# Performance work log

Hardware: AMD Instinct MI355X
Metric: run time of the kernel (lower is better)

Reference implementation:

```python
import jax, jax.numpy as jnp
import numpy as np

I = 1739   # input/output feature size (num_nodes)
H = 256    # hidden size
T = 2048   # trajectory length


def gru(x_seq, h0, W_ih, W_hh, b_ih, b_hh):
    """PyTorch-convention GRU over x_seq [T, I] with h0 [H]. Returns (hs [T,H], h_T [H])."""
    x_proj = x_seq @ W_ih.T + b_ih  # [T, 3H], precompute input projections

    def step(h, xp):
        hh = h @ W_hh.T + b_hh  # [3H]
        xr, xz, xn = xp[:H], xp[H:2 * H], xp[2 * H:]
        hr, hz, hn = hh[:H], hh[H:2 * H], hh[2 * H:]
        r = jax.nn.sigmoid(xr + hr)
        z = jax.nn.sigmoid(xz + hz)
        n = jnp.tanh(xn + r * hn)
        h_new = (1.0 - z) * n + z * h
        return h_new, h_new

    h_T, hs = jax.lax.scan(step, h0, x_proj)
    return hs, h_T


def setup_inputs() -> dict:
    key = jax.random.key(0)
    ks = jax.random.split(key, 12)
    s = 1.0 / np.sqrt(H)
    inp = {
        "input_trajectory": jax.random.normal(ks[0], (1, T, I), jnp.float32),
        "target_trajectory": jax.random.normal(ks[1], (1, T, I), jnp.float32),
        "W_ih_enc": jax.random.uniform(ks[2], (3 * H, I), jnp.float32, -s, s),
        "W_hh_enc": jax.random.uniform(ks[3], (3 * H, H), jnp.float32, -s, s),
        "b_ih_enc": jax.random.uniform(ks[4], (3 * H,), jnp.float32, -s, s),
        "b_hh_enc": jax.random.uniform(ks[5], (3 * H,), jnp.float32, -s, s),
        "W_ih_dec": jax.random.uniform(ks[6], (3 * H, I), jnp.float32, -s, s),
        "W_hh_dec": jax.random.uniform(ks[7], (3 * H, H), jnp.float32, -s, s),
        "b_ih_dec": jax.random.uniform(ks[8], (3 * H,), jnp.float32, -s, s),
        "b_hh_dec": jax.random.uniform(ks[9], (3 * H,), jnp.float32, -s, s),
        "W_out": jax.random.uniform(ks[10], (I, H), jnp.float32, -s, s),
        "b_out": jax.random.uniform(ks[11], (I,), jnp.float32, -s, s),
    }
    return inp


def reference(input_trajectory, target_trajectory,
              W_ih_enc, W_hh_enc, b_ih_enc, b_hh_enc,
              W_ih_dec, W_hh_dec, b_ih_dec, b_hh_dec,
              W_out, b_out):
    x = input_trajectory[0]  # [T, I], batch=1
    h0 = jnp.zeros((H,), x.dtype)
    # Encoder: only the final hidden state is used.
    _, h_enc = gru(x, h0, W_ih_enc, W_hh_enc, b_ih_enc, b_hh_enc)
    # Decoder: loop feeds each input timestep through a 1-step GRU;
    # this is exactly a GRU over the full sequence starting from h_enc.
    hs, _ = gru(x, h_enc, W_ih_dec, W_hh_dec, b_ih_dec, b_hh_dec)  # [T, H]
    # Per-step Linear is a single batched matmul over all steps.
    preds = hs @ W_out.T + b_out  # [T, I]
    # Original cats per-step (1,1,I) tensors along dim=0 -> [T, 1, I].
    return preds[:, None, :]
```

## Files before the change

### kernel.cpp

```cpp
#include <hip/hip_runtime.h>
#include <hip/hip_fp16.h>

#define TT 2048
#define II 1739
#define IIP 1760
#define HN 256
#define H3 768
#define L2E 1.44269504088896f

typedef _Float16 h2 __attribute__((ext_vector_type(2)));
typedef _Float16 h8 __attribute__((ext_vector_type(8)));
typedef float f4 __attribute__((ext_vector_type(4)));

__device__ __forceinline__ float fdot2(h2 a, h2 b, float c) {
#if defined(__has_builtin)
#if __has_builtin(__builtin_amdgcn_fdot2)
  return __builtin_amdgcn_fdot2(a, b, c, false);
#else
  return fmaf((float)a[0], (float)b[0], fmaf((float)a[1], (float)b[1], c));
#endif
#else
  return fmaf((float)a[0], (float)b[0], fmaf((float)a[1], (float)b[1], c));
#endif
}

__device__ __forceinline__ float fast_exp2(float x) {
#if defined(__has_builtin)
#if __has_builtin(__builtin_amdgcn_exp2f)
  return __builtin_amdgcn_exp2f(x);
#else
  return exp2f(x);
#endif
#else
  return exp2f(x);
#endif
}

__device__ __forceinline__ float fast_rcp(float x) {
#if defined(__has_builtin)
#if __has_builtin(__builtin_amdgcn_rcpf)
  return __builtin_amdgcn_rcpf(x);
#else
  return 1.f / x;
#endif
#else
  return 1.f / x;
#endif
}

template <int CTRL>
__device__ __forceinline__ float dpp_qperm(float v) {
  int r = __builtin_amdgcn_update_dpp(0, __builtin_bit_cast(int, v), CTRL, 0xF, 0xF, true);
  return __builtin_bit_cast(float, r);
}

__device__ __forceinline__ h8 h8zero() {
  h8 v;
#pragma unroll
  for (int j = 0; j < 8; ++j) v[j] = (_Float16)0.f;
  return v;
}

#define WSEG (768 * IIP)
#define OSEG (II * HN)
__global__ __launch_bounds__(256) void prep_f16(
    const float* __restrict__ We, const float* __restrict__ Wd,
    const float* __restrict__ Wo,
    _Float16* __restrict__ weh, _Float16* __restrict__ wdh,
    _Float16* __restrict__ woh) {
  const int total = 2 * WSEG + OSEG;
  for (int i = blockIdx.x * 256 + threadIdx.x; i < total; i += gridDim.x * 256) {
    if (i < WSEG) {
      int r = i / IIP, k = i - r * IIP;
      weh[i] = (k < II) ? (_Float16)We[(size_t)r * II + k] : (_Float16)0.f;
    } else if (i < 2 * WSEG) {
      int j = i - WSEG;
      int r = j / IIP, k = j - r * IIP;
      wdh[j] = (k < II) ? (_Float16)Wd[(size_t)r * II + k] : (_Float16)0.f;
    } else {
      int j = i - 2 * WSEG;
      woh[j] = (_Float16)Wo[j];
    }
  }
}

__global__ __launch_bounds__(256) void gemm16(
    const float* __restrict__ A, int K,
    const _Float16* __restrict__ B16, int N, int Kp,
    const float* __restrict__ bias1, const float* __restrict__ bias2, int b2lim,
    float s_lo, float s_hi, int slim,
    float* __restrict__ C) {
  __shared__ _Float16 As[64][40];
  __shared__ _Float16 Bs[64][40];
  const int tid = threadIdx.x;
  const int w = tid >> 6, lane = tid & 63;
  const int col = lane & 15, kg = lane >> 4;
  const int m0 = blockIdx.y * 64, n0 = blockIdx.x * 64;
  const int srow = tid >> 2, skq = tid & 3;
  f4 acc[4];
#pragma unroll
  for (int m = 0; m < 4; ++m) acc[m] = f4{0.f, 0.f, 0.f, 0.f};

  for (int k0 = 0; k0 < Kp; k0 += 32) {
    const int kk = k0 + skq * 8;
    h8 av = h8zero(), bv = h8zero();
    {
      const float* ap = A + (size_t)(m0 + srow) * K + kk;
      if (kk + 8 <= K) {
        float4 f0, f1;
        __builtin_memcpy(&f0, ap, 16);
        __builtin_memcpy(&f1, ap + 4, 16);
        av[0] = (_Float16)f0.x; av[1] = (_Float16)f0.y;
        av[2] = (_Float16)f0.z; av[3] = (_Float16)f0.w;
        av[4] = (_Float16)f1.x; av[5] = (_Float16)f1.y;
        av[6] = (_Float16)f1.z; av[7] = (_Float16)f1.w;
      } else if (kk < K) {
#pragma unroll
        for (int j = 0; j < 8; ++j)
          if (kk + j < K) av[j] = (_Float16)ap[j];
      }
    }
    {
      const int bn = n0 + srow;
      if (bn < N) bv = *(const h8*)(B16 + (size_t)bn * Kp + kk);
    }
    __syncthreads();
    *(h8*)&As[srow][skq * 8] = av;
    *(h8*)&Bs[srow][skq * 8] = bv;
    __syncthreads();
    h8 b = *(const h8*)&Bs[w * 16 + col][kg * 8];
#pragma unroll
    for (int m = 0; m < 4; ++m) {
      h8 a = *(const h8*)&As[m * 16 + col][kg * 8];
      acc[m] = __builtin_amdgcn_mfma_f32_16x16x32_f16(a, b, acc[m], 0, 0, 0);
    }
  }

  const int n = n0 + w * 16 + col;
  if (n < N) {
    float bb = bias1[n];
    if (bias2 && n < b2lim) bb += bias2[n];
    const float s = (n < slim) ? s_lo : s_hi;
#pragma unroll
    for (int m = 0; m < 4; ++m) {
      const int mr = m0 + m * 16 + kg * 4;
#pragma unroll
      for (int r = 0; r < 4; ++r)
        C[(size_t)(mr + r) * N + n] = (acc[m][r] + bb) * s;
    }
  }
}

__global__ __launch_bounds__(512) void gru_seq(
    const float* __restrict__ xp,
    const float* __restrict__ Whh,
    const float* __restrict__ bhh,
    const float* __restrict__ h0,
    float* __restrict__ hs_out,
    float* __restrict__ hT_out) {
  __shared__ __align__(16) uint hbufd[2][160];

  const int tid = threadIdx.x;
  const int lane = tid & 63;
  const int wv = tid >> 6;
  const int kc = lane & 3;
  const int q = wv * 16 + (lane >> 2);
  const int u0 = 2 * q;

  h2 wreg[6][32];
#pragma unroll
  for (int uu = 0; uu < 2; ++uu) {
#pragma unroll
    for (int gg = 0; gg < 3; ++gg) {
      const float sc = (gg == 2) ? (2.f * L2E) : L2E;
      const float* wr = Whh + (size_t)(u0 + uu + gg * HN) * HN + kc * 64;
#pragma unroll
      for (int p = 0; p < 32; ++p) {
        float2 f = *(const float2*)(wr + 2 * p);
        wreg[uu * 3 + gg][p] = h2{(_Float16)(f.x * sc), (_Float16)(f.y * sc)};
      }
    }
  }

  float hj0 = h0 ? h0[u0] : 0.f;
  float hj1 = h0 ? h0[u0 + 1] : 0.f;
  const float bhn0 = bhh[2 * HN + u0] * (2.f * L2E);
  const float bhn1 = bhh[2 * HN + u0 + 1] * (2.f * L2E);

  if (tid < 128) {
    float a = h0 ? h0[2 * tid] : 0.f;
    float b = h0 ? h0[2 * tid + 1] : 0.f;
    h2 pv = h2{(_Float16)a, (_Float16)b};
    hbufd[0][(tid >> 5) * 40 + (tid & 31)] = __builtin_bit_cast(uint, pv);
  }
  __syncthreads();

  const int wadr = (q >> 5) * 40 + (q & 31);

  for (int t = 0; t < TT; ++t) {
    float2 xr, xz, xn;
    {
      const float* xpt = xp + (size_t)t * H3 + u0;
      xr = *(const float2*)(xpt);
      xz = *(const float2*)(xpt + HN);
      xn = *(const float2*)(xpt + 2 * HN);
    }

    const uint* hb = &hbufd[t & 1][kc * 40];
    float a[6] = {0.f, 0.f, 0.f, 0.f, 0.f, 0.f};
#pragma unroll
    for (int qq = 0; qq < 8; ++qq) {
      uint4 v = *(const uint4*)&hb[qq * 4];
      uint hwv[4] = {v.x, v.y, v.z, v.w};
#pragma unroll
      for (int i = 0; i < 6; ++i)
#pragma unroll
        for (int p = 0; p < 4; ++p)
          a[i] = fdot2(wreg[i][qq * 4 + p], __builtin_bit_cast(h2, hwv[p]), a[i]);
    }

#pragma unroll
    for (int i = 0; i < 6; ++i) {
      float v = a[i];
      v += dpp_qperm<0xB1>(v);
      v += dpp_qperm<0x4E>(v);
      a[i] = v;
    }

    float r0 = fast_rcp(1.f + fast_exp2(-(xr.x + a[0])));
    float z0 = fast_rcp(1.f + fast_exp2(-(xz.x + a[1])));
    float n0 = fmaf(2.f, fast_rcp(1.f + fast_exp2(-fmaf(r0, a[2] + bhn0, xn.x))), -1.f);
    hj0 = fmaf(z0, hj0 - n0, n0);
    float r1 = fast_rcp(1.f + fast_exp2(-(xr.y + a[3])));
    float z1 = fast_rcp(1.f + fast_exp2(-(xz.y + a[4])));
    float n1 = fmaf(2.f, fast_rcp(1.f + fast_exp2(-fmaf(r1, a[5] + bhn1, xn.y))), -1.f);
    hj1 = fmaf(z1, hj1 - n1, n1);

    h2 pv = h2{(_Float16)hj0, (_Float16)hj1};
    if (kc == 0) {
      hbufd[(t & 1) ^ 1][wadr] = __builtin_bit_cast(uint, pv);
      if (hs_out) *(float2*)&hs_out[(size_t)t * HN + u0] = make_float2(hj0, hj1);
    }
    __syncthreads();
  }
  if (hT_out && kc == 0) *(float2*)&hT_out[u0] = make_float2(hj0, hj1);
}

extern "C" void kernel_launch(void* const* d_in, const int* in_sizes, int n_in,
                              void* d_out, int out_size, void* d_ws, size_t ws_size,
                              hipStream_t stream) {
  const float* x     = (const float*)d_in[0];
  const float* Wih_e = (const float*)d_in[2];
  const float* Whh_e = (const float*)d_in[3];
  const float* bih_e = (const float*)d_in[4];
  const float* bhh_e = (const float*)d_in[5];
  const float* Wih_d = (const float*)d_in[6];
  const float* Whh_d = (const float*)d_in[7];
  const float* bih_d = (const float*)d_in[8];
  const float* bhh_d = (const float*)d_in[9];
  const float* Wout  = (const float*)d_in[10];
  const float* bout  = (const float*)d_in[11];
  float* out = (float*)d_out;

  float* ws = (float*)d_ws;
  float* xpe  = ws;
  float* xpd  = xpe + (size_t)TT * H3;
  float* hs   = xpd + (size_t)TT * H3;
  float* henc = hs + (size_t)TT * HN;
  _Float16* weh = (_Float16*)(henc + HN);
  _Float16* wdh = weh + (size_t)768 * IIP;
  _Float16* woh = wdh + (size_t)768 * IIP;

  prep_f16<<<dim3(1024), dim3(256), 0, stream>>>(Wih_e, Wih_d, Wout,
                                                 weh, wdh, woh);
  gemm16<<<dim3(12, 32), dim3(256), 0, stream>>>(x, II, weh, H3, IIP,
      bih_e, bhh_e, 2 * HN, L2E, 2.f * L2E, 2 * HN, xpe);
  gemm16<<<dim3(12, 32), dim3(256), 0, stream>>>(x, II, wdh, H3, IIP,
      bih_d, bhh_d, 2 * HN, L2E, 2.f * L2E, 2 * HN, xpd);
  gru_seq<<<1, 512, 0, stream>>>(xpe, Whh_e, bhh_e, nullptr, nullptr, henc);
  gru_seq<<<1, 512, 0, stream>>>(xpd, Whh_d, bhh_d, henc, hs, nullptr);
  gemm16<<<dim3(28, 32), dim3(256), 0, stream>>>(hs, HN, woh, II, HN,
      bout, nullptr, 0, 1.f, 1.f, 0, out);
}
```

Before: 4.598 ms.

## Split GRU scan across two workgroups and overlap decoder projection with encoder scan

Measured after the change: 7.875 ms. 71.3% more time.

```diff
diff --git a/kernel.cpp b/kernel.cpp
--- a/kernel.cpp
+++ b/kernel.cpp
@@ -84,18 +84,17 @@
   }
 }
 
-__global__ __launch_bounds__(256) void gemm16(
+__device__ __forceinline__ void gemm16_tile(
+    int tid, int bx, int by,
     const float* __restrict__ A, int K,
     const _Float16* __restrict__ B16, int N, int Kp,
     const float* __restrict__ bias1, const float* __restrict__ bias2, int b2lim,
     float s_lo, float s_hi, int slim,
-    float* __restrict__ C) {
-  __shared__ _Float16 As[64][40];
-  __shared__ _Float16 Bs[64][40];
-  const int tid = threadIdx.x;
+    float* __restrict__ C,
+    _Float16 (*As)[40], _Float16 (*Bs)[40]) {
   const int w = tid >> 6, lane = tid & 63;
   const int col = lane & 15, kg = lane >> 4;
-  const int m0 = blockIdx.y * 64, n0 = blockIdx.x * 64;
+  const int m0 = by * 64, n0 = bx * 64;
   const int srow = tid >> 2, skq = tid & 3;
   f4 acc[4];
 #pragma unroll
@@ -151,99 +150,151 @@
   }
 }
 
-__global__ __launch_bounds__(512) void gru_seq(
-    const float* __restrict__ xp,
-    const float* __restrict__ Whh,
-    const float* __restrict__ bhh,
-    const float* __restrict__ h0,
-    float* __restrict__ hs_out,
-    float* __restrict__ hT_out) {
-  __shared__ __align__(16) uint hbufd[2][160];
-
+__global__ __launch_bounds__(256) void gemm16(
+    const float* __restrict__ A, int K,
+    const _Float16* __restrict__ B16, int N, int Kp,
+    const float* __restrict__ bias1, const float* __restrict__ bias2, int b2lim,
+    float s_lo, float s_hi, int slim,
+    float* __restrict__ C) {
+  __shared__ _Float16 As[64][40];
+  __shared__ _Float16 Bs[64][40];
+  gemm16_tile(threadIdx.x, blockIdx.x, blockIdx.y, A, K, B16, N, Kp,
+              bias1, bias2, b2lim, s_lo, s_hi, slim, C, As, Bs);
+}
+
+__device__ void gru_scan2(
+    int b,
+    const float* __restrict__ xp, const float* __restrict__ Whh,
+    const float* __restrict__ bhh, const float* __restrict__ h0,
+    float* __restrict__ hs_out, float* __restrict__ hT_out,
+    uint* __restrict__ slots, uint* __restrict__ flags,
+    uint* hbufd ) {
   const int tid = threadIdx.x;
   const int lane = tid & 63;
   const int wv = tid >> 6;
   const int kc = lane & 3;
   const int q = wv * 16 + (lane >> 2);
-  const int u0 = 2 * q;
-
-  h2 wreg[6][32];
-#pragma unroll
-  for (int uu = 0; uu < 2; ++uu) {
-#pragma unroll
-    for (int gg = 0; gg < 3; ++gg) {
-      const float sc = (gg == 2) ? (2.f * L2E) : L2E;
-      const float* wr = Whh + (size_t)(u0 + uu + gg * HN) * HN + kc * 64;
-#pragma unroll
-      for (int p = 0; p < 32; ++p) {
-        float2 f = *(const float2*)(wr + 2 * p);
-        wreg[uu * 3 + gg][p] = h2{(_Float16)(f.x * sc), (_Float16)(f.y * sc)};
-      }
-    }
-  }
-
-  float hj0 = h0 ? h0[u0] : 0.f;
-  float hj1 = h0 ? h0[u0 + 1] : 0.f;
-  const float bhn0 = bhh[2 * HN + u0] * (2.f * L2E);
-  const float bhn1 = bhh[2 * HN + u0 + 1] * (2.f * L2E);
-
-  if (tid < 128) {
-    float a = h0 ? h0[2 * tid] : 0.f;
-    float b = h0 ? h0[2 * tid + 1] : 0.f;
-    h2 pv = h2{(_Float16)a, (_Float16)b};
-    hbufd[0][(tid >> 5) * 40 + (tid & 31)] = __builtin_bit_cast(uint, pv);
+  const int u = 128 * b + q;
+  const int peer = 1 - b;
+  uint* myflag = flags + b * 64;
+  uint* pflag = flags + peer * 64;
+
+  h2 wreg[3][32];
+#pragma unroll
+  for (int gg = 0; gg < 3; ++gg) {
+    const float sc = (gg == 2) ? (2.f * L2E) : L2E;
+    const float* wr = Whh + (size_t)(gg * HN + u) * HN + kc * 64;
+#pragma unroll
+    for (int p = 0; p < 32; ++p) {
+      float2 f = *(const float2*)(wr + 2 * p);
+      wreg[gg][p] = h2{(_Float16)(f.x * sc), (_Float16)(f.y * sc)};
+    }
+  }
+
+  float hj = h0 ? h0[u] : 0.f;
+  const float bhn = bhh[2 * HN + u] * (2.f * L2E);
+
+  if (tid < 64) {
+    const int d = 64 * b + tid;
+    float a = h0 ? h0[2 * d] : 0.f;
+    float c = h0 ? h0[2 * d + 1] : 0.f;
+    h2 pv = h2{(_Float16)a, (_Float16)c};
+    uint pw = __builtin_bit_cast(uint, pv);
+    hbufd[(d >> 5) * 40 + (d & 31)] = pw;
+    __hip_atomic_store(&slots[b * 64 + tid], pw, __ATOMIC_RELAXED,
+                       __HIP_MEMORY_SCOPE_AGENT);
   }
   __syncthreads();
-
-  const int wadr = (q >> 5) * 40 + (q & 31);
+  if (tid == 0)
+    __hip_atomic_store(myflag, 1u, __ATOMIC_RELEASE, __HIP_MEMORY_SCOPE_AGENT);
 
   for (int t = 0; t < TT; ++t) {
-    float2 xr, xz, xn;
-    {
-      const float* xpt = xp + (size_t)t * H3 + u0;
-      xr = *(const float2*)(xpt);
-      xz = *(const float2*)(xpt + HN);
-      xn = *(const float2*)(xpt + 2 * HN);
-    }
-
-    const uint* hb = &hbufd[t & 1][kc * 40];
-    float a[6] = {0.f, 0.f, 0.f, 0.f, 0.f, 0.f};
+    const int cur = (t & 1) * 160, nxt = ((t + 1) & 1) * 160;
+    if (wv == 0) {
+      while (__hip_atomic_load(pflag, __ATOMIC_ACQUIRE,
+                               __HIP_MEMORY_SCOPE_AGENT) < (uint)(t + 1))
+        __builtin_amdgcn_s_sleep(1);
+      const int dr = 64 * peer + lane;
+      uint d = __hip_atomic_load(&slots[(t & 1) * 128 + peer * 64 + lane],
+                                 __ATOMIC_RELAXED, __HIP_MEMORY_SCOPE_AGENT);
+      hbufd[cur + (dr >> 5) * 40 + (dr & 31)] = d;
+    }
+    __syncthreads();
+
+    const float* xpt = xp + (size_t)t * H3 + u;
+    float xr = xpt[0], xz = xpt[HN], xn = xpt[2 * HN];
+
+    const uint* hb = &hbufd[cur + kc * 40];
+    float a0 = 0.f, a1 = 0.f, a2 = 0.f;
 #pragma unroll
     for (int qq = 0; qq < 8; ++qq) {
       uint4 v = *(const uint4*)&hb[qq * 4];
-      uint hwv[4] = {v.x, v.y, v.z, v.w};
-#pragma unroll
-      for (int i = 0; i < 6; ++i)
-#pragma unroll
-        for (int p = 0; p < 4; ++p)
-          a[i] = fdot2(wreg[i][qq * 4 + p], __builtin_bit_cast(h2, hwv[p]), a[i]);
-    }
-
-#pragma unroll
-    for (int i = 0; i < 6; ++i) {
-      float v = a[i];
-      v += dpp_qperm<0xB1>(v);
-      v += dpp_qperm<0x4E>(v);
-      a[i] = v;
-    }
-
-    float r0 = fast_rcp(1.f + fast_exp2(-(xr.x + a[0])));
-    float z0 = fast_rcp(1.f + fast_exp2(-(xz.x + a[1])));
-    float n0 = fmaf(2.f, fast_rcp(1.f + fast_exp2(-fmaf(r0, a[2] + bhn0, xn.x))), -1.f);
-    hj0 = fmaf(z0, hj0 - n0, n0);
-    float r1 = fast_rcp(1.f + fast_exp2(-(xr.y + a[3])));
-    float z1 = fast_rcp(1.f + fast_exp2(-(xz.y + a[4])));
-    float n1 = fmaf(2.f, fast_rcp(1.f + fast_exp2(-fmaf(r1, a[5] + bhn1, xn.y))), -1.f);
-    hj1 = fmaf(z1, hj1 - n1, n1);
-
-    h2 pv = h2{(_Float16)hj0, (_Float16)hj1};
-    if (kc == 0) {
-      hbufd[(t & 1) ^ 1][wadr] = __builtin_bit_cast(uint, pv);
-      if (hs_out) *(float2*)&hs_out[(size_t)t * HN + u0] = make_float2(hj0, hj1);
+      uint hv[4] = {v.x, v.y, v.z, v.w};
+#pragma unroll
+      for (int p = 0; p < 4; ++p) {
+        h2 hp = __builtin_bit_cast(h2, hv[p]);
+        a0 = fdot2(wreg[0][qq * 4 + p], hp, a0);
+        a1 = fdot2(wreg[1][qq * 4 + p], hp, a1);
+        a2 = fdot2(wreg[2][qq * 4 + p], hp, a2);
+      }
+    }
+    a0 += dpp_qperm<0xB1>(a0); a0 += dpp_qperm<0x4E>(a0);
+    a1 += dpp_qperm<0xB1>(a1); a1 += dpp_qperm<0x4E>(a1);
+    a2 += dpp_qperm<0xB1>(a2); a2 += dpp_qperm<0x4E>(a2);
+
+    float r = fast_rcp(1.f + fast_exp2(-(xr + a0)));
+    float z = fast_rcp(1.f + fast_exp2(-(xz + a1)));
+    float nv = fmaf(2.f, fast_rcp(1.f + fast_exp2(-fmaf(r, a2 + bhn, xn))), -1.f);
+    hj = fmaf(z, hj - nv, nv);
+
+    float hj4 = __shfl(hj, lane + 4);
+    if ((lane & 7) == 0) {
+      h2 pv = h2{(_Float16)hj, (_Float16)hj4};
+      uint pw = __builtin_bit_cast(uint, pv);
+      const int ld = wv * 8 + (lane >> 3);
+      const int dg = 64 * b + ld;
+      hbufd[nxt + (dg >> 5) * 40 + (dg & 31)] = pw;
+      __hip_atomic_store(&slots[((t + 1) & 1) * 128 + b * 64 + ld], pw,
+                         __ATOMIC_RELAXED, __HIP_MEMORY_SCOPE_AGENT);
+      if (hs_out) *(float2*)&hs_out[(size_t)t * HN + u] = make_float2(hj, hj4);
     }
     __syncthreads();
-  }
-  if (hT_out && kc == 0) *(float2*)&hT_out[u0] = make_float2(hj0, hj1);
+    if (tid == 0)
+      __hip_atomic_store(myflag, (uint)(t + 2), __ATOMIC_RELEASE,
+                         __HIP_MEMORY_SCOPE_AGENT);
+  }
+  float hj4t = __shfl(hj, lane + 4);
+  if (hT_out && (lane & 7) == 0)
+    *(float2*)&hT_out[u] = make_float2(hj, hj4t);
+}
+
+__global__ __launch_bounds__(512) void gru_pair(
+    const float* __restrict__ xp, const float* __restrict__ Whh,
+    const float* __restrict__ bhh, const float* __restrict__ h0,
+    float* __restrict__ hs_out, float* __restrict__ hT_out,
+    uint* __restrict__ slots, uint* __restrict__ flags) {
+  __shared__ __align__(16) uint hbufd[2 * 160];
+  gru_scan2(blockIdx.x, xp, Whh, bhh, h0, hs_out, hT_out, slots, flags, hbufd);
+}
+
+__global__ __launch_bounds__(512) void fused_enc(
+    const float* __restrict__ xpe, const float* __restrict__ Whh_e,
+    const float* __restrict__ bhh_e, float* __restrict__ henc,
+    uint* __restrict__ slots, uint* __restrict__ flags,
+    const float* __restrict__ x, const _Float16* __restrict__ wdh,
+    const float* __restrict__ bih_d, const float* __restrict__ bhh_d,
+    float* __restrict__ xpd) {
+  __shared__ __align__(16) uint hbufd[2 * 160];
+  __shared__ _Float16 As[64][40];
+  __shared__ _Float16 Bs[64][40];
+  if (blockIdx.x < 2) {
+    gru_scan2(blockIdx.x, xpe, Whh_e, bhh_e, nullptr, nullptr, henc,
+              slots, flags, hbufd);
+  } else {
+    const int bb = blockIdx.x - 2;
+    gemm16_tile(threadIdx.x & 255, bb % 12, bb / 12, x, II, wdh, H3, IIP,
+                bih_d, bhh_d, 2 * HN, L2E, 2.f * L2E, 2 * HN, xpd, As, Bs);
+  }
 }
 
 extern "C" void kernel_launch(void* const* d_in, const int* in_sizes, int n_in,
@@ -270,15 +321,21 @@
   _Float16* weh = (_Float16*)(henc + HN);
   _Float16* wdh = weh + (size_t)768 * IIP;
   _Float16* woh = wdh + (size_t)768 * IIP;
+  uint* sync = (uint*)(woh + (size_t)II * HN);
+  uint* slots_e = sync;
+  uint* slots_d = sync + 256;
+  uint* flags   = sync + 512;
+
+  hipMemsetAsync(flags, 0, 256 * sizeof(uint), stream);
 
   prep_f16<<<dim3(1024), dim3(256), 0, stream>>>(Wih_e, Wih_d, Wout,
                                                  weh, wdh, woh);
   gemm16<<<dim3(12, 32), dim3(256), 0, stream>>>(x, II, weh, H3, IIP,
       bih_e, bhh_e, 2 * HN, L2E, 2.f * L2E, 2 * HN, xpe);
-  gemm16<<<dim3(12, 32), dim3(256), 0, stream>>>(x, II, wdh, H3, IIP,
-      bih_d, bhh_d, 2 * HN, L2E, 2.f * L2E, 2 * HN, xpd);
-  gru_seq<<<1, 512, 0, stream>>>(xpe, Whh_e, bhh_e, nullptr, nullptr, henc);
-  gru_seq<<<1, 512, 0, stream>>>(xpd, Whh_d, bhh_d, henc, hs, nullptr);
+  fused_enc<<<dim3(386), dim3(512), 0, stream>>>(xpe, Whh_e, bhh_e, henc,
+      slots_e, flags, x, wdh, bih_d, bhh_d, xpd);
+  gru_pair<<<dim3(2), dim3(512), 0, stream>>>(xpd, Whh_d, bhh_d, henc,
+      hs, nullptr, slots_d, flags + 128);
   gemm16<<<dim3(28, 32), dim3(256), 0, stream>>>(hs, HN, woh, II, HN,
       bout, nullptr, 0, 1.f, 1.f, 0, out);
 }
```

## Overlap decoder input-projection GEMM with encoder GRU scan in one launch

Applied to the files above, without the earlier changes.

Result: slower. 5.108 ms (+11.1%).

```diff
diff --git a/kernel.cpp b/kernel.cpp
--- a/kernel.cpp
+++ b/kernel.cpp
@@ -84,18 +84,17 @@
   }
 }
 
-__global__ __launch_bounds__(256) void gemm16(
+__device__ __forceinline__ void gemm16_tile(
+    int tid, int bx, int by,
     const float* __restrict__ A, int K,
     const _Float16* __restrict__ B16, int N, int Kp,
     const float* __restrict__ bias1, const float* __restrict__ bias2, int b2lim,
     float s_lo, float s_hi, int slim,
-    float* __restrict__ C) {
-  __shared__ _Float16 As[64][40];
-  __shared__ _Float16 Bs[64][40];
-  const int tid = threadIdx.x;
+    float* __restrict__ C,
+    _Float16 (*As)[40], _Float16 (*Bs)[40]) {
   const int w = tid >> 6, lane = tid & 63;
   const int col = lane & 15, kg = lane >> 4;
-  const int m0 = blockIdx.y * 64, n0 = blockIdx.x * 64;
+  const int m0 = by * 64, n0 = bx * 64;
   const int srow = tid >> 2, skq = tid & 3;
   f4 acc[4];
 #pragma unroll
@@ -151,15 +150,26 @@
   }
 }
 
-__global__ __launch_bounds__(512) void gru_seq(
+__global__ __launch_bounds__(256) void gemm16(
+    const float* __restrict__ A, int K,
+    const _Float16* __restrict__ B16, int N, int Kp,
+    const float* __restrict__ bias1, const float* __restrict__ bias2, int b2lim,
+    float s_lo, float s_hi, int slim,
+    float* __restrict__ C) {
+  __shared__ _Float16 As[64][40];
+  __shared__ _Float16 Bs[64][40];
+  gemm16_tile(threadIdx.x, blockIdx.x, blockIdx.y, A, K, B16, N, Kp,
+              bias1, bias2, b2lim, s_lo, s_hi, slim, C, As, Bs);
+}
+
+__device__ void gru_scan(
     const float* __restrict__ xp,
     const float* __restrict__ Whh,
     const float* __restrict__ bhh,
     const float* __restrict__ h0,
     float* __restrict__ hs_out,
-    float* __restrict__ hT_out) {
-  __shared__ __align__(16) uint hbufd[2][160];
-
+    float* __restrict__ hT_out,
+    uint* hbufd ) {
   const int tid = threadIdx.x;
   const int lane = tid & 63;
   const int wv = tid >> 6;
@@ -191,13 +201,14 @@
     float a = h0 ? h0[2 * tid] : 0.f;
     float b = h0 ? h0[2 * tid + 1] : 0.f;
     h2 pv = h2{(_Float16)a, (_Float16)b};
-    hbufd[0][(tid >> 5) * 40 + (tid & 31)] = __builtin_bit_cast(uint, pv);
+    hbufd[(tid >> 5) * 40 + (tid & 31)] = __builtin_bit_cast(uint, pv);
   }
   __syncthreads();
 
   const int wadr = (q >> 5) * 40 + (q & 31);
 
   for (int t = 0; t < TT; ++t) {
+    const int cur = (t & 1) * 160, nxt = ((t + 1) & 1) * 160;
     float2 xr, xz, xn;
     {
       const float* xpt = xp + (size_t)t * H3 + u0;
@@ -206,7 +217,7 @@
       xn = *(const float2*)(xpt + 2 * HN);
     }
 
-    const uint* hb = &hbufd[t & 1][kc * 40];
+    const uint* hb = &hbufd[cur + kc * 40];
     float a[6] = {0.f, 0.f, 0.f, 0.f, 0.f, 0.f};
 #pragma unroll
     for (int qq = 0; qq < 8; ++qq) {
@@ -238,12 +249,38 @@
 
     h2 pv = h2{(_Float16)hj0, (_Float16)hj1};
     if (kc == 0) {
-      hbufd[(t & 1) ^ 1][wadr] = __builtin_bit_cast(uint, pv);
+      hbufd[nxt + wadr] = __builtin_bit_cast(uint, pv);
       if (hs_out) *(float2*)&hs_out[(size_t)t * HN + u0] = make_float2(hj0, hj1);
     }
     __syncthreads();
   }
   if (hT_out && kc == 0) *(float2*)&hT_out[u0] = make_float2(hj0, hj1);
+}
+
+__global__ __launch_bounds__(512) void gru_seq(
+    const float* __restrict__ xp, const float* __restrict__ Whh,
+    const float* __restrict__ bhh, const float* __restrict__ h0,
+    float* __restrict__ hs_out, float* __restrict__ hT_out) {
+  __shared__ __align__(16) uint hbufd[2 * 160];
+  gru_scan(xp, Whh, bhh, h0, hs_out, hT_out, hbufd);
+}
+
+__global__ __launch_bounds__(512) void fused_enc(
+    const float* __restrict__ xpe, const float* __restrict__ Whh_e,
+    const float* __restrict__ bhh_e, float* __restrict__ henc,
+    const float* __restrict__ x, const _Float16* __restrict__ wdh,
+    const float* __restrict__ bih_d, const float* __restrict__ bhh_d,
+    float* __restrict__ xpd) {
+  __shared__ __align__(16) uint hbufd[2 * 160];
+  __shared__ _Float16 As[64][40];
+  __shared__ _Float16 Bs[64][40];
+  if (blockIdx.x == 0) {
+    gru_scan(xpe, Whh_e, bhh_e, nullptr, nullptr, henc, hbufd);
+  } else {
+    const int bb = blockIdx.x - 1;
+    gemm16_tile(threadIdx.x & 255, bb % 12, bb / 12, x, II, wdh, H3, IIP,
+                bih_d, bhh_d, 2 * HN, L2E, 2.f * L2E, 2 * HN, xpd, As, Bs);
+  }
 }
 
 extern "C" void kernel_launch(void* const* d_in, const int* in_sizes, int n_in,
@@ -275,9 +312,8 @@
                                                  weh, wdh, woh);
   gemm16<<<dim3(12, 32), dim3(256), 0, stream>>>(x, II, weh, H3, IIP,
       bih_e, bhh_e, 2 * HN, L2E, 2.f * L2E, 2 * HN, xpe);
-  gemm16<<<dim3(12, 32), dim3(256), 0, stream>>>(x, II, wdh, H3, IIP,
-      bih_d, bhh_d, 2 * HN, L2E, 2.f * L2E, 2 * HN, xpd);
-  gru_seq<<<1, 512, 0, stream>>>(xpe, Whh_e, bhh_e, nullptr, nullptr, henc);
+  fused_enc<<<dim3(385), dim3(512), 0, stream>>>(xpe, Whh_e, bhh_e, henc,
+                                                 x, wdh, bih_d, bhh_d, xpd);
   gru_seq<<<1, 512, 0, stream>>>(xpd, Whh_d, bhh_d, henc, hs, nullptr);
   gemm16<<<dim3(28, 32), dim3(256), 0, stream>>>(hs, HN, woh, II, HN,
       bout, nullptr, 0, 1.f, 1.f, 0, out);
```
